# Optimization experiments

Hardware: AMD Instinct MI355X
Metric: run time of the kernel (lower is better)

## Reference

```python
import jax, jax.numpy as jnp
import numpy as np

DIM = 768  # N, feature length and Linear dim
B, C = 16, 1024  # batch, token count


def setup_inputs() -> dict:
    key = jax.random.key(0)
    ks = jax.random.split(key, 7)
    s = 1.0 / np.sqrt(DIM)
    return {
        "x": jax.random.normal(ks[0], (B, C, DIM), dtype=jnp.float32),
        "Wq": jax.random.uniform(ks[1], (DIM, DIM), jnp.float32, -s, s),
        "bq": jax.random.uniform(ks[2], (DIM,), jnp.float32, -s, s),
        "Wk": jax.random.uniform(ks[3], (DIM, DIM), jnp.float32, -s, s),
        "bk": jax.random.uniform(ks[4], (DIM,), jnp.float32, -s, s),
        "Wv": jax.random.uniform(ks[5], (DIM, DIM), jnp.float32, -s, s),
        "bv": jax.random.uniform(ks[6], (DIM,), jnp.float32, -s, s),
    }


def reference(x, Wq, bq, Wk, bk, Wv, bv):
    # x: [B, C, N] with N == DIM; Linears act on last axis (torch y = x W^T + b)
    Bb, Cc, N = x.shape
    q = jnp.einsum("bcn,dn->bcd", x, Wq) + bq
    k = jnp.einsum("bcn,dn->bcd", x, Wk) + bk
    v = jnp.einsum("bcn,dn->bcd", x, Wv) + bv
    attn = jax.nn.softmax(jnp.einsum("bcd,bed->bce", q, k) * (N ** -0.5), axis=-1)  # [B,C,C]
    out = jnp.einsum("bce,ben->bcn", attn, v)  # [B,C,N]
    # faithful to torch: transpose(1,2) then reshape back to (B,C,N) -- a buffer reinterpretation
    out = jnp.transpose(out, (0, 2, 1)).reshape(Bb, Cc, N)
    return out + x  # dropout is identity at inference
```

## Files before the change

### kernel.cpp

```cpp
#include <hip/hip_runtime.h>
#include <hip/hip_bf16.h>

typedef __bf16 v8bf __attribute__((ext_vector_type(8)));
typedef float f32x4 __attribute__((ext_vector_type(4)));

static __device__ __forceinline__ unsigned short f2b(float f){
  union { float f; unsigned int u; } c; c.f = f;
  return (unsigned short)((c.u + 0x7FFFu + ((c.u >> 16) & 1u)) >> 16);
}
static __device__ __forceinline__ float b2f(unsigned int h){
  union { unsigned int u; float f; } c; c.u = h << 16; return c.f;
}

static __device__ __forceinline__ void gld_lds16(const void* g, void* l){
  __builtin_amdgcn_global_load_lds(
      (const __attribute__((address_space(1))) unsigned int*)g,
      (__attribute__((address_space(3))) unsigned int*)l, 16, 0, 0);
}

#define FENCE __builtin_amdgcn_sched_barrier(0)

template<int NW, bool DEEP>
static __device__ __forceinline__ void gemmcore(
    const unsigned short* __restrict__ A, int lda,
    const unsigned short* __restrict__ B, int ldb,
    int NT, unsigned short* smem, f32x4 acc[8][NW])
{
  const int tid  = threadIdx.x;
  const int lane = tid & 63;
  const int w    = tid >> 6;
  const int wr   = w >> 2, wc = w & 3;
  const int lr   = lane & 15, lg = lane >> 4;
  char* sm = (char*)smem;
  constexpr int NAB   = DEEP ? 3 : 2;
  constexpr int BBASE = NAB * 32768;
  constexpr int BBUF  = NW * 8192;

  #pragma unroll
  for (int m=0;m<8;++m)
    #pragma unroll
    for (int n=0;n<NW;++n)
      acc[m][n] = (f32x4){0.f,0.f,0.f,0.f};

  const int rloc = tid >> 3;
  const int scol = ((tid & 7) ^ ((tid >> 3) & 7)) << 3;
  const unsigned short* Ab0 = A + (size_t)rloc*lda + scol;
  const unsigned short* Bb0 = B + (size_t)rloc*ldb + scol;

  auto stA = [&](int ab, int i, int kE){
    gld_lds16(Ab0 + (size_t)(i*64)*lda + kE, sm + ab*32768 + i*8192 + w*1024);
  };
  auto stB = [&](int db, int i, int kE){
    gld_lds16(Bb0 + (size_t)(i*64)*ldb + kE, sm + BBASE + db*BBUF + i*8192 + w*1024);
  };

  const int ce0 = (((lg*8))      ^ ((lr&7)<<3)) * 2;
  const int ce1 = (((32 + lg*8)) ^ ((lr&7)<<3)) * 2;

  v8bf bX[NW][2], bY[NW][2], af0[2][2], af1[2][2];

  auto rdA = [&](v8bf (&dst)[2][2], char* base, int qq){
    #pragma unroll
    for (int mm=0;mm<2;++mm){
      char* rp = base + ((qq*2+mm)*16+lr)*128;
      dst[mm][0] = *(const v8bf*)(rp + ce0);
      dst[mm][1] = *(const v8bf*)(rp + ce1);
    }
  };
  auto rdB = [&](v8bf (&dst)[NW][2], char* base){
    #pragma unroll
    for (int n=0;n<NW;++n){
      char* rp = base + (n*16+lr)*128;
      dst[n][0] = *(const v8bf*)(rp + ce0);
      dst[n][1] = *(const v8bf*)(rp + ce1);
    }
  };
  auto domfma = [&](v8bf (&a)[2][2], v8bf (&bb)[NW][2], int qq){
    __builtin_amdgcn_s_setprio(1);
    #pragma unroll
    for (int mm=0;mm<2;++mm)
      #pragma unroll
      for (int n=0;n<NW;++n){
        acc[qq*2+mm][n] = __builtin_amdgcn_mfma_f32_16x16x32_bf16(a[mm][0], bb[n][0], acc[qq*2+mm][n], 0,0,0);
        acc[qq*2+mm][n] = __builtin_amdgcn_mfma_f32_16x16x32_bf16(a[mm][1], bb[n][1], acc[qq*2+mm][n], 0,0,0);
      }
    __builtin_amdgcn_s_setprio(0);
  };

  auto ktile = [&](int kt, int ar, int an, int as,
                   v8bf (&bc)[NW][2], v8bf (&bn)[NW][2]){
    char* Ab = sm + ar*32768 + wr*16384;
    char* An = sm + an*32768 + wr*16384;
    char* Bn = sm + BBASE + ((kt+1)&1)*BBUF + wc*(NW*2048);
    const int kAraw = DEEP ? kt+2 : kt+1;
    const int kA = (kAraw < NT ? kAraw : NT-1)*64;
    const int kB = (kt+2 < NT ? kt+2 : NT-1)*64;
    const int db = kt & 1;

    stA(as,0,kA); stA(as,1,kA);
    rdA(af1, Ab, 1);
    FENCE; asm volatile("s_waitcnt lgkmcnt(4)" ::: "memory"); FENCE;
    domfma(af0, bc, 0);
    __builtin_amdgcn_s_barrier();

    stA(as,2,kA); stA(as,3,kA);
    rdA(af0, Ab, 2);
    FENCE; asm volatile("s_waitcnt lgkmcnt(4)" ::: "memory"); FENCE;
    domfma(af1, bc, 1);
    __builtin_amdgcn_s_barrier();

    stB(db,0,kB); stB(db,1,kB);
    rdA(af1, Ab, 3);
    FENCE; asm volatile("s_waitcnt lgkmcnt(4)" ::: "memory"); FENCE;
    domfma(af0, bc, 2);
    if constexpr (DEEP) asm volatile("s_waitcnt vmcnt(6)" ::: "memory");
    else                asm volatile("s_waitcnt vmcnt(2)" ::: "memory");
    __builtin_amdgcn_s_barrier();

    #pragma unroll
    for (int i=2;i<NW;++i) stB(db,i,kB);
    rdA(af0, An, 0);
    rdB(bn, Bn);
    if constexpr (NW==3) { FENCE; asm volatile("s_waitcnt lgkmcnt(10)" ::: "memory"); FENCE; }
    else                 { FENCE; asm volatile("s_waitcnt lgkmcnt(12)" ::: "memory"); FENCE; }
    domfma(af1, bc, 3);
    __builtin_amdgcn_s_barrier();
  };

  #pragma unroll
  for (int i=0;i<4;++i)  stA(0,i,0);
  #pragma unroll
  for (int i=0;i<NW;++i) stB(0,i,0);
  if constexpr (DEEP) {
    #pragma unroll
    for (int i=0;i<4;++i) stA(1,i,64);
  }
  #pragma unroll
  for (int i=0;i<NW;++i) stB(1,i,64);
  if constexpr (DEEP)      asm volatile("s_waitcnt vmcnt(7)" ::: "memory");
  else if constexpr (NW==3) asm volatile("s_waitcnt vmcnt(3)" ::: "memory");
  else                      asm volatile("s_waitcnt vmcnt(4)" ::: "memory");
  __builtin_amdgcn_s_barrier();
  rdB(bX, sm + BBASE + wc*(NW*2048));
  rdA(af0, sm + wr*16384, 0);

  if constexpr (DEEP) {
    int c0 = 0;
    for (int kt = 0; kt < NT; kt += 2) {
      const int c1 = (c0+1==3) ? 0 : c0+1;
      const int c2 = (c1+1==3) ? 0 : c1+1;
      ktile(kt,   c0, c1, c2, bX, bY);
      ktile(kt+1, c1, c2, c0, bY, bX);
      c0 = c2;
    }
  } else {
    for (int kt = 0; kt < NT; kt += 2) {
      ktile(kt,   0, 1, 1, bX, bY);
      ktile(kt+1, 1, 0, 0, bY, bX);
    }
  }
}

__global__ __launch_bounds__(256) void convert_kernel(
    const float* __restrict__ x,
    const float* __restrict__ Wq, const float* __restrict__ Wk,
    const float* __restrict__ Wv,
    unsigned short* __restrict__ Xb, unsigned short* __restrict__ Wb)
{
  const int NX = 3145728;
  const int NW_ = 147456;
  const int total = NX + 3*NW_;
  for (int i = blockIdx.x*256 + threadIdx.x; i < total; i += gridDim.x*256) {
    const float* src; unsigned short* dst; int off;
    if (i < NX) { src = x; dst = Xb; off = i; }
    else {
      int j = i - NX; int z = j / NW_; off = j - z*NW_;
      src = (z==0) ? Wq : ((z==1) ? Wk : Wv);
      dst = Wb + (size_t)z*589824;
    }
    float4 v = reinterpret_cast<const float4*>(src)[off];
    ushort4 h; h.x=f2b(v.x); h.y=f2b(v.y); h.z=f2b(v.z); h.w=f2b(v.w);
    reinterpret_cast<ushort4*>(dst)[off] = h;
  }
}

__global__ __launch_bounds__(512, 2) void qkv_kernel(
    const unsigned short* __restrict__ Xb, const unsigned short* __restrict__ Wb,
    const float* __restrict__ bq, const float* __restrict__ bk,
    const float* __restrict__ bv,
    unsigned short* __restrict__ Qb, unsigned short* __restrict__ Kb,
    unsigned short* __restrict__ Vt)
{
  extern __shared__ unsigned short smem[];
  const int bid = blockIdx.x;
  const int wg  = (bid & 7)*96 + (bid >> 3);
  const int mt  = wg / 12, nt = wg % 12;

  f32x4 acc[8][3];
  gemmcore<3,true>(Xb + (size_t)mt*256*768, 768,
                   Wb + (size_t)nt*192*768, 768, 12, smem, acc);

  const int tid = threadIdx.x, lane = tid & 63, w = tid >> 6;
  const int wr = w >> 2, wc = w & 3, lr = lane & 15, lg = lane >> 4;
  const int z = nt >> 2;
  const float* bias = (z==0) ? bq : ((z==1) ? bk : bv);
  const int colbase = (nt & 3)*192 + wc*48;

  if (z < 2) {
    unsigned short* dst = (z==0) ? Qb : Kb;
    #pragma unroll
    for (int m=0;m<8;++m){
      int row0 = mt*256 + wr*128 + m*16 + lg*4;
      #pragma unroll
      for (int n=0;n<3;++n){
        int col = colbase + n*16 + lr;
        float bb = bias[col];
        #pragma unroll
        for (int r=0;r<4;++r)
          dst[(size_t)(row0+r)*768 + col] = f2b(acc[m][n][r] + bb);
      }
    }
  } else {
    const int rowG0 = mt*256;
    const int batch = rowG0 >> 10;
    const int ebase = rowG0 & 1023;
    unsigned short* dst = Vt + (size_t)batch*786432;
    #pragma unroll
    for (int m=0;m<8;++m){
      int e0 = ebase + wr*128 + m*16 + lg*4;
      #pragma unroll
      for (int n=0;n<3;++n){
        int col = colbase + n*16 + lr;
        float bb = bias[col];
        ushort4 h;
        h.x = f2b(acc[m][n][0] + bb);
        h.y = f2b(acc[m][n][1] + bb);
        h.z = f2b(acc[m][n][2] + bb);
        h.w = f2b(acc[m][n][3] + bb);
        *reinterpret_cast<ushort4*>(dst + (size_t)col*1024 + e0) = h;
      }
    }
  }
}

__global__ __launch_bounds__(512, 2) void scores_kernel(
    const unsigned short* __restrict__ Qb,
    const unsigned short* __restrict__ Kb,
    unsigned short* __restrict__ Eb)
{
  extern __shared__ unsigned short smem[];
  const int mt = blockIdx.x, nt = blockIdx.y, b = blockIdx.z;

  f32x4 acc[8][4];
  gemmcore<4,false>(Qb + (size_t)b*786432 + (size_t)mt*256*768, 768,
                    Kb + (size_t)b*786432 + (size_t)nt*256*768, 768,
                    12, smem, acc);

  const float scale = 0.03608439182435161f;
  const int tid = threadIdx.x, lane = tid & 63, w = tid >> 6;
  const int wr = w >> 2, wc = w & 3, lr = lane & 15, lg = lane >> 4;
  unsigned short* dst = Eb + (size_t)b*1048576;
  #pragma unroll
  for (int m=0;m<8;++m){
    int row0 = mt*256 + wr*128 + m*16 + lg*4;
    #pragma unroll
    for (int n=0;n<4;++n){
      int col = nt*256 + wc*64 + n*16 + lr;
      #pragma unroll
      for (int r=0;r<4;++r)
        dst[(size_t)(row0+r)*1024 + col] = f2b(__expf(acc[m][n][r] * scale));
    }
  }
}

__global__ __launch_bounds__(256) void rowsum_kernel(
    const unsigned short* __restrict__ E, float* __restrict__ D)
{
  int row  = blockIdx.x*4 + (threadIdx.x >> 6);
  int lane = threadIdx.x & 63;
  const unsigned short* p = E + (size_t)row*1024 + lane*16;
  uint4 v0 = *reinterpret_cast<const uint4*>(p);
  uint4 v1 = *reinterpret_cast<const uint4*>(p + 8);
  unsigned int uu[8] = {v0.x, v0.y, v0.z, v0.w, v1.x, v1.y, v1.z, v1.w};
  float s = 0.f;
  #pragma unroll
  for (int i=0;i<8;++i){ s += b2f(uu[i] & 0xffffu); s += b2f(uu[i] >> 16); }
  #pragma unroll
  for (int off=1; off<64; off<<=1) s += __shfl_xor(s, off, 64);
  if (lane == 0) D[row] = s;
}

__global__ __launch_bounds__(512, 2) void pv_kernel(
    const unsigned short* __restrict__ Eb,
    const unsigned short* __restrict__ Vt,
    const float* __restrict__ D,
    const float* __restrict__ x, float* __restrict__ out)
{
  extern __shared__ unsigned short smem[];
  const int mt = blockIdx.x, nt = blockIdx.y, b = blockIdx.z;

  f32x4 acc[8][3];
  gemmcore<3,true>(Eb + (size_t)b*1048576 + (size_t)mt*256*1024, 1024,
                   Vt + (size_t)b*786432  + (size_t)nt*192*1024, 1024,
                   16, smem, acc);

  const int tid = threadIdx.x, lane = tid & 63, w = tid >> 6;
  const int wr = w >> 2, wc = w & 3, lr = lane & 15, lg = lane >> 4;
  const float* xb = x   + (size_t)b*786432;
  float*       ob = out + (size_t)b*786432;
  const float* Db = D + b*1024;
  #pragma unroll
  for (int m=0;m<8;++m){
    int c0 = mt*256 + wr*128 + m*16 + lg*4;
    float inv0 = 1.0f / Db[c0+0];
    float inv1 = 1.0f / Db[c0+1];
    float inv2 = 1.0f / Db[c0+2];
    float inv3 = 1.0f / Db[c0+3];
    #pragma unroll
    for (int n=0;n<3;++n){
      int col = nt*192 + wc*48 + n*16 + lr;
      size_t idx = (size_t)col*1024 + c0;
      float4 xv = *reinterpret_cast<const float4*>(xb + idx);
      float4 o;
      o.x = acc[m][n][0]*inv0 + xv.x;
      o.y = acc[m][n][1]*inv1 + xv.y;
      o.z = acc[m][n][2]*inv2 + xv.z;
      o.w = acc[m][n][3]*inv3 + xv.w;
      *reinterpret_cast<float4*>(ob + idx) = o;
    }
  }
}

extern "C" void kernel_launch(void* const* d_in, const int* in_sizes, int n_in,
                              void* d_out, int out_size, void* d_ws, size_t ws_size,
                              hipStream_t stream)
{
  const float* x  = (const float*)d_in[0];
  const float* Wq = (const float*)d_in[1];
  const float* bq = (const float*)d_in[2];
  const float* Wk = (const float*)d_in[3];
  const float* bk = (const float*)d_in[4];
  const float* Wv = (const float*)d_in[5];
  const float* bv = (const float*)d_in[6];
  float* out = (float*)d_out;

  char* ws = (char*)d_ws;
  unsigned short* Xb = (unsigned short*)(ws);
  unsigned short* Wb = (unsigned short*)(ws + 25165824);
  unsigned short* Eb = (unsigned short*)(ws);
  unsigned short* Qb = (unsigned short*)(ws + 33554432);
  float*          Dd = (float*)         (ws + 33554432);
  unsigned short* Kb = (unsigned short*)(ws + 58720256);
  unsigned short* Vt = (unsigned short*)(ws + 83886080);

  convert_kernel<<<dim3(2048),     dim3(256), 0,      stream>>>(x, Wq, Wk, Wv, Xb, Wb);
  qkv_kernel    <<<dim3(768),      dim3(512), 147456, stream>>>(Xb, Wb, bq, bk, bv, Qb, Kb, Vt);
  scores_kernel <<<dim3(4, 4, 16), dim3(512), 131072, stream>>>(Qb, Kb, Eb);
  rowsum_kernel <<<dim3(4096),     dim3(256), 0,      stream>>>(Eb, Dd);
  pv_kernel     <<<dim3(4, 4, 16), dim3(512), 147456, stream>>>(Eb, Vt, Dd, x, out);
}
```

Before: 158.6 us.

## Use 128-row QKV tiles with smaller LDS and remap attention blocks per XCD

Adds a dedicated 128x192 GEMM core with a double-buffered 80KB LDS footprint for the QKV projection. This doubles the block count to 1536 and raises the launch bounds, aiming for better occupancy and a better-balanced wave count across CUs. The scores and PV kernels switch to a flat 1D grid with a swizzle that places two batches per XCD, so blocks sharing Q/K/V data land on the same L2. Smaller tiles raise the global traffic per FLOP for QKV, and the remap relies on round-robin dispatch of blocks across XCDs.

After: 144.4 us. -8.9%, faster.

```diff
diff --git a/kernel.cpp b/kernel.cpp
--- a/kernel.cpp
+++ b/kernel.cpp
@@ -19,6 +19,79 @@
 }
 
 #define FENCE __builtin_amdgcn_sched_barrier(0)
+
+static __device__ __forceinline__ void gemm128(
+    const unsigned short* __restrict__ A, int lda,
+    const unsigned short* __restrict__ B, int ldb,
+    int NT, unsigned short* smem, f32x4 acc[4][3])
+{
+  const int tid  = threadIdx.x;
+  const int lane = tid & 63;
+  const int w    = tid >> 6;
+  const int wr   = w >> 2, wc = w & 3;
+  const int lr   = lane & 15, lg = lane >> 4;
+  char* sm = (char*)smem;
+
+  #pragma unroll
+  for (int m=0;m<4;++m)
+    #pragma unroll
+    for (int n=0;n<3;++n)
+      acc[m][n] = (f32x4){0.f,0.f,0.f,0.f};
+
+  const int rloc = tid >> 3;
+  const int scol = ((tid & 7) ^ ((tid >> 3) & 7)) << 3;
+  const unsigned short* Ab0 = A + (size_t)rloc*lda + scol;
+  const unsigned short* Bb0 = B + (size_t)rloc*ldb + scol;
+
+  auto stA = [&](int d, int i, int kE){
+    gld_lds16(Ab0 + (size_t)(i*64)*lda + kE, sm + d*16384 + i*8192 + w*1024);
+  };
+  auto stB = [&](int d, int i, int kE){
+    gld_lds16(Bb0 + (size_t)(i*64)*ldb + kE, sm + 32768 + d*24576 + i*8192 + w*1024);
+  };
+
+  const int ce0 = (((lg*8))      ^ ((lr&7)<<3)) * 2;
+  const int ce1 = (((32 + lg*8)) ^ ((lr&7)<<3)) * 2;
+
+  stA(0,0,0); stA(0,1,0);
+  stB(0,0,0); stB(0,1,0); stB(0,2,0);
+  asm volatile("s_waitcnt vmcnt(0)" ::: "memory");
+  __builtin_amdgcn_s_barrier();
+
+  for (int kt = 0; kt < NT; ++kt) {
+    const int d  = kt & 1;
+    const int kN = (kt+1 < NT ? kt+1 : NT-1)*64;
+    stA(d^1,0,kN); stA(d^1,1,kN);
+    stB(d^1,0,kN); stB(d^1,1,kN); stB(d^1,2,kN);
+    v8bf a[4][2], b[3][2];
+    char* Abase = sm + d*16384;
+    char* Bbase = sm + 32768 + d*24576;
+    #pragma unroll
+    for (int m=0;m<4;++m){
+      char* rp = Abase + (wr*64 + m*16 + lr)*128;
+      a[m][0] = *(const v8bf*)(rp + ce0);
+      a[m][1] = *(const v8bf*)(rp + ce1);
+    }
+    #pragma unroll
+    for (int n=0;n<3;++n){
+      char* rp = Bbase + (wc*48 + n*16 + lr)*128;
+      b[n][0] = *(const v8bf*)(rp + ce0);
+      b[n][1] = *(const v8bf*)(rp + ce1);
+    }
+    FENCE; asm volatile("s_waitcnt lgkmcnt(0)" ::: "memory"); FENCE;
+    __builtin_amdgcn_s_setprio(1);
+    #pragma unroll
+    for (int m=0;m<4;++m)
+      #pragma unroll
+      for (int n=0;n<3;++n){
+        acc[m][n] = __builtin_amdgcn_mfma_f32_16x16x32_bf16(a[m][0], b[n][0], acc[m][n], 0,0,0);
+        acc[m][n] = __builtin_amdgcn_mfma_f32_16x16x32_bf16(a[m][1], b[n][1], acc[m][n], 0,0,0);
+      }
+    __builtin_amdgcn_s_setprio(0);
+    asm volatile("s_waitcnt vmcnt(0)" ::: "memory");
+    __builtin_amdgcn_s_barrier();
+  }
+}
 
 template<int NW, bool DEEP>
 static __device__ __forceinline__ void gemmcore(
@@ -184,7 +257,7 @@
   }
 }
 
-__global__ __launch_bounds__(512, 2) void qkv_kernel(
+__global__ __launch_bounds__(512, 4) void qkv_kernel(
     const unsigned short* __restrict__ Xb, const unsigned short* __restrict__ Wb,
     const float* __restrict__ bq, const float* __restrict__ bk,
     const float* __restrict__ bv,
@@ -193,12 +266,12 @@
 {
   extern __shared__ unsigned short smem[];
   const int bid = blockIdx.x;
-  const int wg  = (bid & 7)*96 + (bid >> 3);
+  const int wg  = (bid & 7)*192 + (bid >> 3);
   const int mt  = wg / 12, nt = wg % 12;
 
-  f32x4 acc[8][3];
-  gemmcore<3,true>(Xb + (size_t)mt*256*768, 768,
-                   Wb + (size_t)nt*192*768, 768, 12, smem, acc);
+  f32x4 acc[4][3];
+  gemm128(Xb + (size_t)mt*128*768, 768,
+          Wb + (size_t)nt*192*768, 768, 12, smem, acc);
 
   const int tid = threadIdx.x, lane = tid & 63, w = tid >> 6;
   const int wr = w >> 2, wc = w & 3, lr = lane & 15, lg = lane >> 4;
@@ -209,8 +282,8 @@
   if (z < 2) {
     unsigned short* dst = (z==0) ? Qb : Kb;
     #pragma unroll
-    for (int m=0;m<8;++m){
-      int row0 = mt*256 + wr*128 + m*16 + lg*4;
+    for (int m=0;m<4;++m){
+      int row0 = mt*128 + wr*64 + m*16 + lg*4;
       #pragma unroll
       for (int n=0;n<3;++n){
         int col = colbase + n*16 + lr;
@@ -221,13 +294,12 @@
       }
     }
   } else {
-    const int rowG0 = mt*256;
-    const int batch = rowG0 >> 10;
-    const int ebase = rowG0 & 1023;
+    const int batch = mt >> 3;
+    const int ebase = (mt & 7)*128;
     unsigned short* dst = Vt + (size_t)batch*786432;
     #pragma unroll
-    for (int m=0;m<8;++m){
-      int e0 = ebase + wr*128 + m*16 + lg*4;
+    for (int m=0;m<4;++m){
+      int e0 = ebase + wr*64 + m*16 + lg*4;
       #pragma unroll
       for (int n=0;n<3;++n){
         int col = colbase + n*16 + lr;
@@ -249,7 +321,11 @@
     unsigned short* __restrict__ Eb)
 {
   extern __shared__ unsigned short smem[];
-  const int mt = blockIdx.x, nt = blockIdx.y, b = blockIdx.z;
+  const int lid = blockIdx.x;
+  const int seq = lid >> 3;
+  const int b   = (lid & 7)*2 + (seq >> 4);
+  const int t   = seq & 15;
+  const int mt  = t >> 2, nt = t & 3;
 
   f32x4 acc[8][4];
   gemmcore<4,false>(Qb + (size_t)b*786432 + (size_t)mt*256*768, 768,
@@ -297,7 +373,11 @@
     const float* __restrict__ x, float* __restrict__ out)
 {
   extern __shared__ unsigned short smem[];
-  const int mt = blockIdx.x, nt = blockIdx.y, b = blockIdx.z;
+  const int lid = blockIdx.x;
+  const int seq = lid >> 3;
+  const int b   = (lid & 7)*2 + (seq >> 4);
+  const int t   = seq & 15;
+  const int mt  = t >> 2, nt = t & 3;
 
   f32x4 acc[8][3];
   gemmcore<3,true>(Eb + (size_t)b*1048576 + (size_t)mt*256*1024, 1024,
@@ -353,9 +433,9 @@
   unsigned short* Kb = (unsigned short*)(ws + 58720256);
   unsigned short* Vt = (unsigned short*)(ws + 83886080);
 
-  convert_kernel<<<dim3(2048),     dim3(256), 0,      stream>>>(x, Wq, Wk, Wv, Xb, Wb);
-  qkv_kernel    <<<dim3(768),      dim3(512), 147456, stream>>>(Xb, Wb, bq, bk, bv, Qb, Kb, Vt);
-  scores_kernel <<<dim3(4, 4, 16), dim3(512), 131072, stream>>>(Qb, Kb, Eb);
-  rowsum_kernel <<<dim3(4096),     dim3(256), 0,      stream>>>(Eb, Dd);
-  pv_kernel     <<<dim3(4, 4, 16), dim3(512), 147456, stream>>>(Eb, Vt, Dd, x, out);
-}
+  convert_kernel<<<dim3(2048), dim3(256), 0,      stream>>>(x, Wq, Wk, Wv, Xb, Wb);
+  qkv_kernel    <<<dim3(1536), dim3(512), 81920,  stream>>>(Xb, Wb, bq, bk, bv, Qb, Kb, Vt);
+  scores_kernel <<<dim3(256),  dim3(512), 131072, stream>>>(Qb, Kb, Eb);
+  rowsum_kernel <<<dim3(4096), dim3(256), 0,      stream>>>(Eb, Dd);
+  pv_kernel     <<<dim3(256),  dim3(512), 147456, stream>>>(Eb, Vt, Dd, x, out);
+}
```
